# Optimization experiments

Hardware: AMD Instinct MI355X
Metric: run time of the kernel (lower is better)

The kernel has to match this reference:

```python
import jax, jax.numpy as jnp
import numpy as np

EPS = 1e-7
N_NODES = 100000

# --- Lorentz model (c = 1), working at the origin o = (1, 0, ..., 0) ---

def expmap0(v_spatial):
    """Exp map at origin: tangent spatial part [N, d] -> hyperboloid point [N, d+1]."""
    nrm = jnp.sqrt(jnp.maximum(jnp.sum(v_spatial * v_spatial, axis=-1, keepdims=True), EPS))
    x0 = jnp.cosh(nrm)
    xs = jnp.sinh(nrm) / nrm * v_spatial
    return jnp.concatenate([x0, xs], axis=-1)


def logmap0(x):
    """Log map at origin: point [N, d+1] -> tangent spatial part [N, d]."""
    x0 = jnp.maximum(x[..., :1], 1.0 + EPS)
    xs = x[..., 1:]
    nrm = jnp.sqrt(jnp.maximum(jnp.sum(xs * xs, axis=-1, keepdims=True), EPS))
    return jnp.arccosh(x0) / nrm * xs


def sigmoid_nonlin(x):
    # log map -> sigmoid in tangent space -> exp map (c_in = c_out = 1)
    return expmap0(jax.nn.sigmoid(logmap0(x)))


def hgcn_layer(x, edge_index, W, b):
    """HGCN conv: tangent-space linear + mean aggregation over edges + exp map."""
    t = logmap0(x)                      # [N, d_in]
    h = t @ W + b                       # [N, d_out]
    src, dst = edge_index[0], edge_index[1]
    msg = h[src]                        # [E, d_out] gather
    agg = jax.ops.segment_sum(msg, dst, num_segments=N_NODES)
    deg = jax.ops.segment_sum(jnp.ones((edge_index.shape[1],), h.dtype), dst,
                              num_segments=N_NODES)
    agg = agg / jnp.maximum(deg, 1.0)[:, None]
    return expmap0(agg)


def setup_inputs() -> dict:
    key = jax.random.key(0)
    ks = jax.random.split(key, 10)
    d_in, h1, h2, h_mlp, d_out = 64, 64, 64, 128, 40
    return {
        "features": jax.random.normal(ks[0], (N_NODES, d_in), jnp.float32),
        "edge_index": jax.random.randint(ks[1], (2, 1600000), 0, N_NODES, jnp.int64),
        "W1": jax.random.normal(ks[2], (d_in, h1), jnp.float32) * 0.05,
        "b1": jnp.zeros((h1,), jnp.float32),
        "W2": jax.random.normal(ks[3], (h1, h2), jnp.float32) * 0.05,
        "b2": jnp.zeros((h2,), jnp.float32),
        "W3": jax.random.normal(ks[4], (h2, h_mlp), jnp.float32) * 0.05,
        "b3": jnp.zeros((h_mlp,), jnp.float32),
        "W4": jax.random.normal(ks[5], (h_mlp, d_out), jnp.float32) * 0.05,
        "b4": jnp.zeros((d_out,), jnp.float32),
    }


def reference(features, edge_index, W1, b1, W2, b2, W3, b3, W4, b4):
    # lift Euclidean features to the hyperboloid (pad time coord, exp map)
    x = expmap0(features)                       # [N, d_in+1]
    x = hgcn_layer(x, edge_index, W1, b1)
    x = sigmoid_nonlin(x)
    x = hgcn_layer(x, edge_index, W2, b2)
    x = sigmoid_nonlin(x)
    t = logmap0(x)                              # [N, h2] (spatial part, drops time coord)
    # MLP head (dropout inactive at eval)
    h = jax.nn.relu(t @ W3 + b3)
    return h @ W4 + b4
```

## Files before the change

### kernel.cpp

```cpp
#include <hip/hip_runtime.h>


constexpr int CSHIFT = 9;
constexpr int CNODES = 1 << CSHIFT;
constexpr int EPB    = 4096;
constexpr int EPT    = EPB / 256;
constexpr int CAP    = 16384;

constexpr int W1_OFF = 0;
constexpr int W2_OFF = 64 * 72;
constexpr int W3_OFF = W2_OFF + 64 * 72;
constexpr int W4_OFF = W3_OFF + 128 * 72;
constexpr int WIMG_TOT = W4_OFF + 48 * 136;
constexpr int W234_SH = WIMG_TOT - W2_OFF;

typedef __attribute__((ext_vector_type(8))) short short8;
typedef __attribute__((ext_vector_type(4))) float floatx4;

__device__ __forceinline__ float sigmoidf(float x) {
    return 1.0f / (1.0f + __expf(-x));
}
__device__ __forceinline__ unsigned short f2bf(float f) {
    unsigned int u = __float_as_uint(f);
    u = (u + 0x7FFFu + ((u >> 16) & 1u)) >> 16;
    return (unsigned short)u;
}

__global__ __launch_bounds__(256) void cast_k(const float* __restrict__ in,
                                              unsigned short* __restrict__ out,
                                              int n8) {
    int i = blockIdx.x * 256 + threadIdx.x;
    if (i >= n8) return;
    const float4* p = (const float4*)in + (size_t)i * 2;
    float4 a = p[0], b = p[1];
    uint4 o;
    o.x = (unsigned)f2bf(a.x) | ((unsigned)f2bf(a.y) << 16);
    o.y = (unsigned)f2bf(a.z) | ((unsigned)f2bf(a.w) << 16);
    o.z = (unsigned)f2bf(b.x) | ((unsigned)f2bf(b.y) << 16);
    o.w = (unsigned)f2bf(b.z) | ((unsigned)f2bf(b.w) << 16);
    ((uint4*)out)[i] = o;
}

__global__ __launch_bounds__(256) void prep_k(const float* __restrict__ W1,
                                              const float* __restrict__ W2,
                                              const float* __restrict__ W3,
                                              const float* __restrict__ W4,
                                              unsigned short* __restrict__ img) {
    int i = blockIdx.x * 256 + threadIdx.x;
    if (i >= WIMG_TOT) return;
    float v = 0.f;
    if (i < W2_OFF) {
        int j = i, n = j / 72, k = j % 72;
        if (k < 64) v = W1[k * 64 + n];
    } else if (i < W3_OFF) {
        int j = i - W2_OFF, n = j / 72, k = j % 72;
        if (k < 64) v = W2[k * 64 + n];
    } else if (i < W4_OFF) {
        int j = i - W3_OFF, n = j / 72, k = j % 72;
        if (k < 64) v = W3[k * 128 + n];
    } else {
        int j = i - W4_OFF, n = j / 136, k = j % 136;
        if (n < 40 && k < 128) v = W4[k * 40 + n];
    }
    img[i] = f2bf(v);
}

__global__ __launch_bounds__(256) void part_a(const int* __restrict__ src,
                                              const int* __restrict__ dst,
                                              int* __restrict__ ccur,
                                              int* __restrict__ arena,
                                              int E, int NBUCK) {
    __shared__ int  hist[256];
    __shared__ int  exoff[256];
    __shared__ int  lcur[256];
    __shared__ int  gbase[256];
    __shared__ int  stage[EPB];
    __shared__ unsigned char stageB[EPB];

    const int tid = threadIdx.x;
    const int e0  = blockIdx.x * EPB;
    const int ec  = min(EPB, E - e0);

    int pk[EPT], bk[EPT];
    hist[tid] = 0;
    __syncthreads();
    #pragma unroll
    for (int j = 0; j < EPT; j++) {
        int idx = tid + j * 256;
        if (idx < ec) {
            int s = src[e0 + idx];
            int d = dst[e0 + idx];
            bk[j] = d >> CSHIFT;
            pk[j] = s | ((d & (CNODES - 1)) << 17);
            atomicAdd(&hist[bk[j]], 1);
        } else bk[j] = -1;
    }
    __syncthreads();
    const int h = hist[tid];
    exoff[tid] = h;
    __syncthreads();
    for (int dd = 1; dd < 256; dd <<= 1) {
        int v = 0;
        if (tid >= dd) v = exoff[tid - dd];
        __syncthreads();
        if (tid >= dd) exoff[tid] += v;
        __syncthreads();
    }
    const int ex = exoff[tid] - h;
    int gb = 0;
    if (tid < NBUCK && h > 0) gb = atomicAdd(ccur + tid, h);
    __syncthreads();
    exoff[tid] = ex;
    lcur[tid]  = ex;
    gbase[tid] = gb;
    __syncthreads();
    #pragma unroll
    for (int j = 0; j < EPT; j++) {
        if (bk[j] >= 0) {
            int l = atomicAdd(&lcur[bk[j]], 1);
            stage[l]  = pk[j];
            stageB[l] = (unsigned char)bk[j];
        }
    }
    __syncthreads();
    for (int i = tid; i < ec; i += 256) {
        int b = stageB[i];
        arena[(size_t)b * CAP + gbase[b] + (i - exoff[b])] = stage[i];
    }
}

__global__ __launch_bounds__(256) void scanc_k(const int* __restrict__ ccur,
                                               int* __restrict__ coff,
                                               int* __restrict__ offN,
                                               int NBUCK, int E) {
    __shared__ int sh[256];
    const int tid = threadIdx.x;
    sh[tid] = (tid < NBUCK) ? ccur[tid] : 0;
    __syncthreads();
    for (int d = 1; d < 256; d <<= 1) {
        int v = 0;
        if (tid >= d) v = sh[tid - d];
        __syncthreads();
        if (tid >= d) sh[tid] += v;
        __syncthreads();
    }
    if (tid < NBUCK) coff[tid] = (tid > 0) ? sh[tid - 1] : 0;
    if (tid == 0) { coff[NBUCK] = E; *offN = E; }
}

__global__ __launch_bounds__(256) void csr_fine(const int* __restrict__ arena,
                                                const int* __restrict__ coff,
                                                int* __restrict__ off,
                                                int* __restrict__ ssrc, int N) {
    __shared__ int cnt[CNODES];
    __shared__ int cur[CNODES];
    __shared__ int part[256];
    const int b = blockIdx.x;
    const int node0 = b << CSHIFT;
    const int cbeg = coff[b];
    const int ec   = coff[b + 1] - cbeg;
    const int* pe  = arena + (size_t)b * CAP;
    const int tid = threadIdx.x;

    cnt[tid] = 0;
    cnt[tid + 256] = 0;
    __syncthreads();
    for (int i = tid; i < ec; i += 256)
        atomicAdd(&cnt[(pe[i] >> 17) & (CNODES - 1)], 1);
    __syncthreads();
    const int c0 = cnt[2 * tid], c1 = cnt[2 * tid + 1];
    part[tid] = c0 + c1;
    __syncthreads();
    for (int d = 1; d < 256; d <<= 1) {
        int v = 0;
        if (tid >= d) v = part[tid - d];
        __syncthreads();
        if (tid >= d) part[tid] += v;
        __syncthreads();
    }
    const int ex = (tid > 0) ? part[tid - 1] : 0;
    cur[2 * tid]     = ex;
    cur[2 * tid + 1] = ex + c0;
    if (node0 + 2 * tid     < N) off[node0 + 2 * tid]     = cbeg + ex;
    if (node0 + 2 * tid + 1 < N) off[node0 + 2 * tid + 1] = cbeg + ex + c0;
    __syncthreads();
    for (int i = tid; i < ec; i += 256) {
        int p = pe[i];
        int pos = cbeg + atomicAdd(&cur[(p >> 17) & (CNODES - 1)], 1);
        ssrc[pos] = p & 0x1FFFF;
    }
}

#define ACC8(v)                                    \
    acc[0] += __uint_as_float((v).x << 16);        \
    acc[1] += __uint_as_float((v).x & 0xFFFF0000u);\
    acc[2] += __uint_as_float((v).y << 16);        \
    acc[3] += __uint_as_float((v).y & 0xFFFF0000u);\
    acc[4] += __uint_as_float((v).z << 16);        \
    acc[5] += __uint_as_float((v).z & 0xFFFF0000u);\
    acc[6] += __uint_as_float((v).w << 16);        \
    acc[7] += __uint_as_float((v).w & 0xFFFF0000u);

__global__ __launch_bounds__(256) void agg_k(const unsigned short* __restrict__ h,
                                             const int* __restrict__ off,
                                             const int* __restrict__ ssrc,
                                             unsigned short* __restrict__ outb,
                                             int N) {
    int t = blockIdx.x * 256 + threadIdx.x;
    int g = t >> 3;
    if (g >= N) return;
    int q = (t & 7) * 8;
    int beg = off[g], end = off[g + 1];
    float acc[8] = {0.f, 0.f, 0.f, 0.f, 0.f, 0.f, 0.f, 0.f};
    int i = beg;
    for (; i + 4 <= end; i += 4) {
        int s0 = ssrc[i], s1 = ssrc[i + 1], s2 = ssrc[i + 2], s3 = ssrc[i + 3];
        uint4 v0 = *(const uint4*)(h + (size_t)s0 * 64 + q);
        uint4 v1 = *(const uint4*)(h + (size_t)s1 * 64 + q);
        uint4 v2 = *(const uint4*)(h + (size_t)s2 * 64 + q);
        uint4 v3 = *(const uint4*)(h + (size_t)s3 * 64 + q);
        ACC8(v0); ACC8(v1); ACC8(v2); ACC8(v3);
    }
    for (; i < end; i++) {
        int s = ssrc[i];
        uint4 v = *(const uint4*)(h + (size_t)s * 64 + q);
        ACC8(v);
    }
    float inv = 1.0f / (float)max(end - beg, 1);
    uint4 p;
    p.x = (unsigned)f2bf(acc[0] * inv) | ((unsigned)f2bf(acc[1] * inv) << 16);
    p.y = (unsigned)f2bf(acc[2] * inv) | ((unsigned)f2bf(acc[3] * inv) << 16);
    p.z = (unsigned)f2bf(acc[4] * inv) | ((unsigned)f2bf(acc[5] * inv) << 16);
    p.w = (unsigned)f2bf(acc[6] * inv) | ((unsigned)f2bf(acc[7] * inv) << 16);
    *(uint4*)(outb + (size_t)g * 64 + q) = p;
}

__global__ __launch_bounds__(256) void gemmsig_k(
    const unsigned short* __restrict__ Abf, const int* __restrict__ off,
    const unsigned short* __restrict__ img, const float* __restrict__ bias,
    unsigned short* __restrict__ out, int N)
{
    __shared__ alignas(16) unsigned short WT[64 * 72];
    __shared__ float bs[64];
    __shared__ unsigned char dz[64];

    const int tid = threadIdx.x;
    const int rowB = blockIdx.x * 64;
    {
        const uint4* s = (const uint4*)(img + W1_OFF);
        uint4* d = (uint4*)WT;
        #pragma unroll
        for (int i = 0; i < 3; i++) {
            int idx = tid + i * 256;
            if (idx < 576) d[idx] = s[idx];
        }
    }
    if (tid < 64) {
        bs[tid] = bias[tid];
        int row = rowB + tid;
        dz[tid] = (row < N) ? (off[row + 1] == off[row]) : 0;
    }
    __syncthreads();

    const int w = tid >> 6, lane = tid & 63;
    const int m = lane & 15, quad = lane >> 4;
    const int row0 = rowB + w * 16;
    const int arow = min(row0 + m, N - 1);

    floatx4 acc[4];
    #pragma unroll
    for (int c = 0; c < 4; c++) acc[c] = (floatx4){0.f, 0.f, 0.f, 0.f};
    #pragma unroll
    for (int kk = 0; kk < 64; kk += 32) {
        short8 a = *(const short8*)(Abf + (size_t)arow * 64 + kk + quad * 8);
        #pragma unroll
        for (int c = 0; c < 4; c++) {
            short8 b = *(const short8*)(WT + (c * 16 + m) * 72 + kk + quad * 8);
            acc[c] = __builtin_amdgcn_mfma_f32_16x16x32_bf16(a, b, acc[c], 0, 0, 0);
        }
    }
    #pragma unroll
    for (int c = 0; c < 4; c++) {
        int col = c * 16 + m;
        #pragma unroll
        for (int r = 0; r < 4; r++) {
            int rl = w * 16 + quad * 4 + r;
            int row = rowB + rl;
            if (row < N) {
                float v = dz[rl] ? 0.5f : sigmoidf(acc[c][r] + bs[col]);
                out[(size_t)row * 64 + col] = f2bf(v);
            }
        }
    }
}

__global__ __launch_bounds__(256) void ep3b_k(
    const unsigned short* __restrict__ Abf, const int* __restrict__ off,
    const unsigned short* __restrict__ img,
    const float* __restrict__ b2, const float* __restrict__ b3,
    const float* __restrict__ b4, float* __restrict__ out, int N)
{
    __shared__ alignas(16) unsigned short W234[W234_SH];
    __shared__ alignas(16) unsigned short T2[64 * 72];
    __shared__ alignas(16) unsigned short H3[64 * 136];
    __shared__ float b2s[64], b3s[128], b4s[48];
    __shared__ unsigned char dz[64];

    const unsigned short* W2T = W234;
    const unsigned short* W3T = W234 + 64 * 72;
    const unsigned short* W4T = W234 + 64 * 72 + 128 * 72;

    const int tid = threadIdx.x;
    const int rowB = blockIdx.x * 64;
    {
        const uint4* s = (const uint4*)(img + W2_OFF);
        uint4* d = (uint4*)W234;
        for (int i = tid; i < W234_SH / 8; i += 256) d[i] = s[i];
    }
    if (tid < 64) {
        b2s[tid] = b2[tid];
        int row = rowB + tid;
        dz[tid] = (row < N) ? (off[row + 1] == off[row]) : 0;
    }
    if (tid < 128) b3s[tid] = b3[tid];
    if (tid < 48)  b4s[tid] = (tid < 40) ? b4[tid] : 0.f;
    __syncthreads();

    const int w = tid >> 6, lane = tid & 63;
    const int m = lane & 15, quad = lane >> 4;
    const int row0 = rowB + w * 16;

    {
        floatx4 acc[4];
        #pragma unroll
        for (int c = 0; c < 4; c++) acc[c] = (floatx4){0.f, 0.f, 0.f, 0.f};
        const int arow = min(row0 + m, N - 1);
        #pragma unroll
        for (int kk = 0; kk < 64; kk += 32) {
            short8 a = *(const short8*)(Abf + (size_t)arow * 64 + kk + quad * 8);
            #pragma unroll
            for (int c = 0; c < 4; c++) {
                short8 b = *(const short8*)(W2T + (c * 16 + m) * 72 + kk + quad * 8);
                acc[c] = __builtin_amdgcn_mfma_f32_16x16x32_bf16(a, b, acc[c], 0, 0, 0);
            }
        }
        #pragma unroll
        for (int c = 0; c < 4; c++) {
            int col = c * 16 + m;
            #pragma unroll
            for (int r = 0; r < 4; r++) {
                int rl = w * 16 + quad * 4 + r;
                float v = dz[rl] ? 0.5f : sigmoidf(acc[c][r] + b2s[col]);
                T2[rl * 72 + col] = f2bf(v);
            }
        }
    }
    __syncthreads();

    {
        floatx4 acc[8];
        #pragma unroll
        for (int c = 0; c < 8; c++) acc[c] = (floatx4){0.f, 0.f, 0.f, 0.f};
        #pragma unroll
        for (int kk = 0; kk < 64; kk += 32) {
            short8 a = *(const short8*)(T2 + (w * 16 + m) * 72 + kk + quad * 8);
            #pragma unroll
            for (int c = 0; c < 8; c++) {
                short8 b = *(const short8*)(W3T + (c * 16 + m) * 72 + kk + quad * 8);
                acc[c] = __builtin_amdgcn_mfma_f32_16x16x32_bf16(a, b, acc[c], 0, 0, 0);
            }
        }
        #pragma unroll
        for (int c = 0; c < 8; c++) {
            int col = c * 16 + m;
            #pragma unroll
            for (int r = 0; r < 4; r++) {
                int rl = w * 16 + quad * 4 + r;
                H3[rl * 136 + col] = f2bf(fmaxf(acc[c][r] + b3s[col], 0.f));
            }
        }
    }
    __syncthreads();

    {
        floatx4 acc[3];
        #pragma unroll
        for (int c = 0; c < 3; c++) acc[c] = (floatx4){0.f, 0.f, 0.f, 0.f};
        #pragma unroll
        for (int kk = 0; kk < 128; kk += 32) {
            short8 a = *(const short8*)(H3 + (w * 16 + m) * 136 + kk + quad * 8);
            #pragma unroll
            for (int c = 0; c < 3; c++) {
                short8 b = *(const short8*)(W4T + (c * 16 + m) * 136 + kk + quad * 8);
                acc[c] = __builtin_amdgcn_mfma_f32_16x16x32_bf16(a, b, acc[c], 0, 0, 0);
            }
        }
        #pragma unroll
        for (int c = 0; c < 3; c++) {
            int col = c * 16 + m;
            if (col < 40) {
                #pragma unroll
                for (int r = 0; r < 4; r++) {
                    int row = row0 + quad * 4 + r;
                    if (row < N) out[(size_t)row * 40 + col] = acc[c][r] + b4s[col];
                }
            }
        }
    }
}

extern "C" void kernel_launch(void* const* d_in, const int* in_sizes, int n_in,
                              void* d_out, int out_size, void* d_ws, size_t ws_size,
                              hipStream_t stream)
{
    const float* feat = (const float*)d_in[0];
    const int*   eidx = (const int*)d_in[1];
    const float* W1 = (const float*)d_in[2];
    const float* b1 = (const float*)d_in[3];
    const float* W2 = (const float*)d_in[4];
    const float* b2 = (const float*)d_in[5];
    const float* W3 = (const float*)d_in[6];
    const float* b3 = (const float*)d_in[7];
    const float* W4 = (const float*)d_in[8];
    const float* b4 = (const float*)d_in[9];

    const int N = in_sizes[0] / 64;
    const int E = in_sizes[1] / 2;
    const int* src = eidx;
    const int* dst = eidx + E;

    const int NBUCK = (N + CNODES - 1) / CNODES;

    unsigned short* featbf = (unsigned short*)d_ws;
    unsigned short* t1     = featbf + (size_t)N * 64;
    unsigned short* aggF   = t1     + (size_t)N * 64;
    unsigned short* img    = aggF   + (size_t)N * 64;
    int*   off   = (int*)(img + ((WIMG_TOT + 7) & ~7));
    int*   ccur  = off + (N + 1);
    int*   coff  = ccur + NBUCK;
    int*   ssrc  = coff + (NBUCK + 1);
    int*   arena = ssrc + E;
    float* out   = (float*)d_out;

    hipMemsetAsync(ccur, 0, (size_t)NBUCK * sizeof(int), stream);

    const dim3 blk(256);
    const int gP  = (E + EPB - 1) / EPB;
    const int g64 = (N + 63) / 64;
    const int gC  = (N * 64 / 8 + 255) / 256;
    const int gW  = (WIMG_TOT + 255) / 256;
    const int gAg = (int)(((size_t)N * 8 + 255) / 256);

    cast_k<<<gC, blk, 0, stream>>>(feat, featbf, N * 64 / 8);
    prep_k<<<gW, blk, 0, stream>>>(W1, W2, W3, W4, img);
    part_a<<<gP, blk, 0, stream>>>(src, dst, ccur, arena, E, NBUCK);
    scanc_k<<<1, blk, 0, stream>>>(ccur, coff, off + N, NBUCK, E);
    csr_fine<<<NBUCK, blk, 0, stream>>>(arena, coff, off, ssrc, N);

    agg_k<<<gAg, blk, 0, stream>>>(featbf, off, ssrc, aggF, N);
    gemmsig_k<<<g64, blk, 0, stream>>>(aggF, off, img, b1, t1, N);
    agg_k<<<gAg, blk, 0, stream>>>(t1, off, ssrc, aggF, N);
    ep3b_k<<<g64, blk, 0, stream>>>(aggF, off, img, b2, b3, b4, out, N);
}
```

Measured before the change: 246.1 us.

## Merge prep kernels, fold bucket scan into CSR build, pre-swizzle MFMA weights

The feature cast and weight prep now run as one kernel, and the bucket-offset scan is folded into every csr_fine block, which removes two launches. Weights are stored in an MFMA fragment-ready layout and read straight from global memory, so the GEMM kernels no longer stage weights, biases and zero-degree flags in LDS or sync before the first MFMA. The aggregation loop is unrolled to 8 gathers per step with a 2-wide tail to keep more loads in flight. In exchange, every csr_fine block repeats the small scan and the GEMMs depend on L1/L2 hits for their weight reads.

```diff
diff --git a/kernel.cpp b/kernel.cpp
--- a/kernel.cpp
+++ b/kernel.cpp
@@ -7,12 +7,11 @@
 constexpr int EPT    = EPB / 256;
 constexpr int CAP    = 16384;
 
-constexpr int W1_OFF = 0;
-constexpr int W2_OFF = 64 * 72;
-constexpr int W3_OFF = W2_OFF + 64 * 72;
-constexpr int W4_OFF = W3_OFF + 128 * 72;
-constexpr int WIMG_TOT = W4_OFF + 48 * 136;
-constexpr int W234_SH = WIMG_TOT - W2_OFF;
+constexpr int W1F_OFF = 0;
+constexpr int W2F_OFF = 4096;
+constexpr int W3F_OFF = 8192;
+constexpr int W4F_OFF = 16384;
+constexpr int WIMG_TOT = 22528;
 
 typedef __attribute__((ext_vector_type(8))) short short8;
 typedef __attribute__((ext_vector_type(4))) float floatx4;
@@ -26,43 +25,46 @@
     return (unsigned short)u;
 }
 
-__global__ __launch_bounds__(256) void cast_k(const float* __restrict__ in,
-                                              unsigned short* __restrict__ out,
-                                              int n8) {
+__global__ __launch_bounds__(256) void prep_cast_k(
+    const float* __restrict__ feat, unsigned short* __restrict__ featbf,
+    const float* __restrict__ W1, const float* __restrict__ W2,
+    const float* __restrict__ W3, const float* __restrict__ W4,
+    unsigned short* __restrict__ img, int n8)
+{
     int i = blockIdx.x * 256 + threadIdx.x;
-    if (i >= n8) return;
-    const float4* p = (const float4*)in + (size_t)i * 2;
-    float4 a = p[0], b = p[1];
-    uint4 o;
-    o.x = (unsigned)f2bf(a.x) | ((unsigned)f2bf(a.y) << 16);
-    o.y = (unsigned)f2bf(a.z) | ((unsigned)f2bf(a.w) << 16);
-    o.z = (unsigned)f2bf(b.x) | ((unsigned)f2bf(b.y) << 16);
-    o.w = (unsigned)f2bf(b.z) | ((unsigned)f2bf(b.w) << 16);
-    ((uint4*)out)[i] = o;
-}
-
-__global__ __launch_bounds__(256) void prep_k(const float* __restrict__ W1,
-                                              const float* __restrict__ W2,
-                                              const float* __restrict__ W3,
-                                              const float* __restrict__ W4,
-                                              unsigned short* __restrict__ img) {
-    int i = blockIdx.x * 256 + threadIdx.x;
-    if (i >= WIMG_TOT) return;
+    if (i < n8) {
+        const float4* p = (const float4*)feat + (size_t)i * 2;
+        float4 a = p[0], b = p[1];
+        uint4 o;
+        o.x = (unsigned)f2bf(a.x) | ((unsigned)f2bf(a.y) << 16);
+        o.y = (unsigned)f2bf(a.z) | ((unsigned)f2bf(a.w) << 16);
+        o.z = (unsigned)f2bf(b.x) | ((unsigned)f2bf(b.y) << 16);
+        o.w = (unsigned)f2bf(b.z) | ((unsigned)f2bf(b.w) << 16);
+        ((uint4*)featbf)[i] = o;
+        return;
+    }
+    int t = i - n8;
+    if (t >= WIMG_TOT) return;
     float v = 0.f;
-    if (i < W2_OFF) {
-        int j = i, n = j / 72, k = j % 72;
-        if (k < 64) v = W1[k * 64 + n];
-    } else if (i < W3_OFF) {
-        int j = i - W2_OFF, n = j / 72, k = j % 72;
-        if (k < 64) v = W2[k * 64 + n];
-    } else if (i < W4_OFF) {
-        int j = i - W3_OFF, n = j / 72, k = j % 72;
-        if (k < 64) v = W3[k * 128 + n];
+    int s = t;
+    if (s < W2F_OFF) {
+        int j = s & 7, m = (s >> 3) & 15, q = (s >> 7) & 3, kk = (s >> 9) & 1, c = s >> 10;
+        v = W1[(kk * 32 + q * 8 + j) * 64 + c * 16 + m];
+    } else if (s < W3F_OFF) {
+        s -= W2F_OFF;
+        int j = s & 7, m = (s >> 3) & 15, q = (s >> 7) & 3, kk = (s >> 9) & 1, c = s >> 10;
+        v = W2[(kk * 32 + q * 8 + j) * 64 + c * 16 + m];
+    } else if (s < W4F_OFF) {
+        s -= W3F_OFF;
+        int j = s & 7, m = (s >> 3) & 15, q = (s >> 7) & 3, kk = (s >> 9) & 1, c = s >> 10;
+        v = W3[(kk * 32 + q * 8 + j) * 128 + c * 16 + m];
     } else {
-        int j = i - W4_OFF, n = j / 136, k = j % 136;
-        if (n < 40 && k < 128) v = W4[k * 40 + n];
-    }
-    img[i] = f2bf(v);
+        s -= W4F_OFF;
+        int j = s & 7, m = (s >> 3) & 15, q = (s >> 7) & 3, kk = (s >> 9) & 3, c = s >> 11;
+        int n = c * 16 + m;
+        if (n < 40) v = W4[(kk * 32 + q * 8 + j) * 40 + n];
+    }
+    img[t] = f2bf(v);
 }
 
 __global__ __launch_bounds__(256) void part_a(const int* __restrict__ src,
@@ -129,39 +131,33 @@
     }
 }
 
-__global__ __launch_bounds__(256) void scanc_k(const int* __restrict__ ccur,
-                                               int* __restrict__ coff,
-                                               int* __restrict__ offN,
-                                               int NBUCK, int E) {
-    __shared__ int sh[256];
-    const int tid = threadIdx.x;
-    sh[tid] = (tid < NBUCK) ? ccur[tid] : 0;
-    __syncthreads();
-    for (int d = 1; d < 256; d <<= 1) {
-        int v = 0;
-        if (tid >= d) v = sh[tid - d];
-        __syncthreads();
-        if (tid >= d) sh[tid] += v;
-        __syncthreads();
-    }
-    if (tid < NBUCK) coff[tid] = (tid > 0) ? sh[tid - 1] : 0;
-    if (tid == 0) { coff[NBUCK] = E; *offN = E; }
-}
-
 __global__ __launch_bounds__(256) void csr_fine(const int* __restrict__ arena,
-                                                const int* __restrict__ coff,
+                                                const int* __restrict__ ccur,
                                                 int* __restrict__ off,
-                                                int* __restrict__ ssrc, int N) {
+                                                int* __restrict__ ssrc,
+                                                int N, int E, int NBUCK) {
     __shared__ int cnt[CNODES];
     __shared__ int cur[CNODES];
     __shared__ int part[256];
     const int b = blockIdx.x;
     const int node0 = b << CSHIFT;
-    const int cbeg = coff[b];
-    const int ec   = coff[b + 1] - cbeg;
-    const int* pe  = arena + (size_t)b * CAP;
     const int tid = threadIdx.x;
 
+    part[tid] = (tid < NBUCK) ? ccur[tid] : 0;
+    __syncthreads();
+    for (int d = 1; d < 256; d <<= 1) {
+        int v = 0;
+        if (tid >= d) v = part[tid - d];
+        __syncthreads();
+        if (tid >= d) part[tid] += v;
+        __syncthreads();
+    }
+    const int cbeg = (b > 0) ? part[b - 1] : 0;
+    const int ec   = ccur[b];
+    if (b == 0 && tid == 0) off[N] = E;
+    __syncthreads();
+
+    const int* pe = arena + (size_t)b * CAP;
     cnt[tid] = 0;
     cnt[tid + 256] = 0;
     __syncthreads();
@@ -213,17 +209,25 @@
     int beg = off[g], end = off[g + 1];
     float acc[8] = {0.f, 0.f, 0.f, 0.f, 0.f, 0.f, 0.f, 0.f};
     int i = beg;
-    for (; i + 4 <= end; i += 4) {
-        int s0 = ssrc[i], s1 = ssrc[i + 1], s2 = ssrc[i + 2], s3 = ssrc[i + 3];
-        uint4 v0 = *(const uint4*)(h + (size_t)s0 * 64 + q);
-        uint4 v1 = *(const uint4*)(h + (size_t)s1 * 64 + q);
-        uint4 v2 = *(const uint4*)(h + (size_t)s2 * 64 + q);
-        uint4 v3 = *(const uint4*)(h + (size_t)s3 * 64 + q);
+    for (; i + 8 <= end; i += 8) {
+        uint4 v0 = *(const uint4*)(h + (size_t)ssrc[i]     * 64 + q);
+        uint4 v1 = *(const uint4*)(h + (size_t)ssrc[i + 1] * 64 + q);
+        uint4 v2 = *(const uint4*)(h + (size_t)ssrc[i + 2] * 64 + q);
+        uint4 v3 = *(const uint4*)(h + (size_t)ssrc[i + 3] * 64 + q);
+        uint4 v4 = *(const uint4*)(h + (size_t)ssrc[i + 4] * 64 + q);
+        uint4 v5 = *(const uint4*)(h + (size_t)ssrc[i + 5] * 64 + q);
+        uint4 v6 = *(const uint4*)(h + (size_t)ssrc[i + 6] * 64 + q);
+        uint4 v7 = *(const uint4*)(h + (size_t)ssrc[i + 7] * 64 + q);
         ACC8(v0); ACC8(v1); ACC8(v2); ACC8(v3);
+        ACC8(v4); ACC8(v5); ACC8(v6); ACC8(v7);
+    }
+    for (; i + 2 <= end; i += 2) {
+        uint4 v0 = *(const uint4*)(h + (size_t)ssrc[i]     * 64 + q);
+        uint4 v1 = *(const uint4*)(h + (size_t)ssrc[i + 1] * 64 + q);
+        ACC8(v0); ACC8(v1);
     }
     for (; i < end; i++) {
-        int s = ssrc[i];
-        uint4 v = *(const uint4*)(h + (size_t)s * 64 + q);
+        uint4 v = *(const uint4*)(h + (size_t)ssrc[i] * 64 + q);
         ACC8(v);
     }
     float inv = 1.0f / (float)max(end - beg, 1);
@@ -240,55 +244,42 @@
     const unsigned short* __restrict__ img, const float* __restrict__ bias,
     unsigned short* __restrict__ out, int N)
 {
-    __shared__ alignas(16) unsigned short WT[64 * 72];
-    __shared__ float bs[64];
-    __shared__ unsigned char dz[64];
-
     const int tid = threadIdx.x;
     const int rowB = blockIdx.x * 64;
-    {
-        const uint4* s = (const uint4*)(img + W1_OFF);
-        uint4* d = (uint4*)WT;
-        #pragma unroll
-        for (int i = 0; i < 3; i++) {
-            int idx = tid + i * 256;
-            if (idx < 576) d[idx] = s[idx];
-        }
-    }
-    if (tid < 64) {
-        bs[tid] = bias[tid];
-        int row = rowB + tid;
-        dz[tid] = (row < N) ? (off[row + 1] == off[row]) : 0;
-    }
-    __syncthreads();
-
     const int w = tid >> 6, lane = tid & 63;
     const int m = lane & 15, quad = lane >> 4;
     const int row0 = rowB + w * 16;
     const int arow = min(row0 + m, N - 1);
+    const short8* Wf = (const short8*)(img + W1F_OFF);
 
     floatx4 acc[4];
     #pragma unroll
     for (int c = 0; c < 4; c++) acc[c] = (floatx4){0.f, 0.f, 0.f, 0.f};
     #pragma unroll
-    for (int kk = 0; kk < 64; kk += 32) {
-        short8 a = *(const short8*)(Abf + (size_t)arow * 64 + kk + quad * 8);
+    for (int kk = 0; kk < 2; kk++) {
+        short8 a = *(const short8*)(Abf + (size_t)arow * 64 + kk * 32 + quad * 8);
         #pragma unroll
         for (int c = 0; c < 4; c++) {
-            short8 b = *(const short8*)(WT + (c * 16 + m) * 72 + kk + quad * 8);
+            short8 b = Wf[((c * 2 + kk) * 4 + quad) * 16 + m];
             acc[c] = __builtin_amdgcn_mfma_f32_16x16x32_bf16(a, b, acc[c], 0, 0, 0);
         }
+    }
+    bool dzr[4];
+    int rows[4];
+    #pragma unroll
+    for (int r = 0; r < 4; r++) {
+        rows[r] = row0 + quad * 4 + r;
+        dzr[r] = (rows[r] < N) ? (off[rows[r] + 1] == off[rows[r]]) : false;
     }
     #pragma unroll
     for (int c = 0; c < 4; c++) {
         int col = c * 16 + m;
+        float bv = bias[col];
         #pragma unroll
         for (int r = 0; r < 4; r++) {
-            int rl = w * 16 + quad * 4 + r;
-            int row = rowB + rl;
-            if (row < N) {
-                float v = dz[rl] ? 0.5f : sigmoidf(acc[c][r] + bs[col]);
-                out[(size_t)row * 64 + col] = f2bf(v);
+            if (rows[r] < N) {
+                float v = dzr[r] ? 0.5f : sigmoidf(acc[c][r] + bv);
+                out[(size_t)rows[r] * 64 + col] = f2bf(v);
             }
         }
     }
@@ -300,57 +291,44 @@
     const float* __restrict__ b2, const float* __restrict__ b3,
     const float* __restrict__ b4, float* __restrict__ out, int N)
 {
-    __shared__ alignas(16) unsigned short W234[W234_SH];
     __shared__ alignas(16) unsigned short T2[64 * 72];
     __shared__ alignas(16) unsigned short H3[64 * 136];
-    __shared__ float b2s[64], b3s[128], b4s[48];
-    __shared__ unsigned char dz[64];
-
-    const unsigned short* W2T = W234;
-    const unsigned short* W3T = W234 + 64 * 72;
-    const unsigned short* W4T = W234 + 64 * 72 + 128 * 72;
 
     const int tid = threadIdx.x;
     const int rowB = blockIdx.x * 64;
-    {
-        const uint4* s = (const uint4*)(img + W2_OFF);
-        uint4* d = (uint4*)W234;
-        for (int i = tid; i < W234_SH / 8; i += 256) d[i] = s[i];
-    }
-    if (tid < 64) {
-        b2s[tid] = b2[tid];
-        int row = rowB + tid;
-        dz[tid] = (row < N) ? (off[row + 1] == off[row]) : 0;
-    }
-    if (tid < 128) b3s[tid] = b3[tid];
-    if (tid < 48)  b4s[tid] = (tid < 40) ? b4[tid] : 0.f;
-    __syncthreads();
-
     const int w = tid >> 6, lane = tid & 63;
     const int m = lane & 15, quad = lane >> 4;
     const int row0 = rowB + w * 16;
 
     {
+        const short8* Wf = (const short8*)(img + W2F_OFF);
         floatx4 acc[4];
         #pragma unroll
         for (int c = 0; c < 4; c++) acc[c] = (floatx4){0.f, 0.f, 0.f, 0.f};
         const int arow = min(row0 + m, N - 1);
         #pragma unroll
-        for (int kk = 0; kk < 64; kk += 32) {
-            short8 a = *(const short8*)(Abf + (size_t)arow * 64 + kk + quad * 8);
+        for (int kk = 0; kk < 2; kk++) {
+            short8 a = *(const short8*)(Abf + (size_t)arow * 64 + kk * 32 + quad * 8);
             #pragma unroll
             for (int c = 0; c < 4; c++) {
-                short8 b = *(const short8*)(W2T + (c * 16 + m) * 72 + kk + quad * 8);
+                short8 b = Wf[((c * 2 + kk) * 4 + quad) * 16 + m];
                 acc[c] = __builtin_amdgcn_mfma_f32_16x16x32_bf16(a, b, acc[c], 0, 0, 0);
             }
+        }
+        bool dzr[4];
+        #pragma unroll
+        for (int r = 0; r < 4; r++) {
+            int row = row0 + quad * 4 + r;
+            dzr[r] = (row < N) ? (off[row + 1] == off[row]) : false;
         }
         #pragma unroll
         for (int c = 0; c < 4; c++) {
             int col = c * 16 + m;
+            float bv = b2[col];
             #pragma unroll
             for (int r = 0; r < 4; r++) {
                 int rl = w * 16 + quad * 4 + r;
-                float v = dz[rl] ? 0.5f : sigmoidf(acc[c][r] + b2s[col]);
+                float v = dzr[r] ? 0.5f : sigmoidf(acc[c][r] + bv);
                 T2[rl * 72 + col] = f2bf(v);
             }
         }
@@ -358,40 +336,43 @@
     __syncthreads();
 
     {
+        const short8* Wf = (const short8*)(img + W3F_OFF);
         floatx4 acc[8];
         #pragma unroll
         for (int c = 0; c < 8; c++) acc[c] = (floatx4){0.f, 0.f, 0.f, 0.f};
         #pragma unroll
-        for (int kk = 0; kk < 64; kk += 32) {
-            short8 a = *(const short8*)(T2 + (w * 16 + m) * 72 + kk + quad * 8);
+        for (int kk = 0; kk < 2; kk++) {
+            short8 a = *(const short8*)(T2 + (w * 16 + m) * 72 + kk * 32 + quad * 8);
             #pragma unroll
             for (int c = 0; c < 8; c++) {
-                short8 b = *(const short8*)(W3T + (c * 16 + m) * 72 + kk + quad * 8);
+                short8 b = Wf[((c * 2 + kk) * 4 + quad) * 16 + m];
                 acc[c] = __builtin_amdgcn_mfma_f32_16x16x32_bf16(a, b, acc[c], 0, 0, 0);
             }
         }
         #pragma unroll
         for (int c = 0; c < 8; c++) {
             int col = c * 16 + m;
+            float bv = b3[col];
             #pragma unroll
             for (int r = 0; r < 4; r++) {
                 int rl = w * 16 + quad * 4 + r;
-                H3[rl * 136 + col] = f2bf(fmaxf(acc[c][r] + b3s[col], 0.f));
+                H3[rl * 136 + col] = f2bf(fmaxf(acc[c][r] + bv, 0.f));
             }
         }
     }
     __syncthreads();
 
     {
+        const short8* Wf = (const short8*)(img + W4F_OFF);
         floatx4 acc[3];
         #pragma unroll
         for (int c = 0; c < 3; c++) acc[c] = (floatx4){0.f, 0.f, 0.f, 0.f};
         #pragma unroll
-        for (int kk = 0; kk < 128; kk += 32) {
-            short8 a = *(const short8*)(H3 + (w * 16 + m) * 136 + kk + quad * 8);
+        for (int kk = 0; kk < 4; kk++) {
+            short8 a = *(const short8*)(H3 + (w * 16 + m) * 136 + kk * 32 + quad * 8);
             #pragma unroll
             for (int c = 0; c < 3; c++) {
-                short8 b = *(const short8*)(W4T + (c * 16 + m) * 136 + kk + quad * 8);
+                short8 b = Wf[((c * 4 + kk) * 4 + quad) * 16 + m];
                 acc[c] = __builtin_amdgcn_mfma_f32_16x16x32_bf16(a, b, acc[c], 0, 0, 0);
             }
         }
@@ -399,10 +380,11 @@
         for (int c = 0; c < 3; c++) {
             int col = c * 16 + m;
             if (col < 40) {
+                float bv = b4[col];
                 #pragma unroll
                 for (int r = 0; r < 4; r++) {
                     int row = row0 + quad * 4 + r;
-                    if (row < N) out[(size_t)row * 40 + col] = acc[c][r] + b4s[col];
+                    if (row < N) out[(size_t)row * 40 + col] = acc[c][r] + bv;
                 }
             }
         }
@@ -435,10 +417,9 @@
     unsigned short* t1     = featbf + (size_t)N * 64;
     unsigned short* aggF   = t1     + (size_t)N * 64;
     unsigned short* img    = aggF   + (size_t)N * 64;
-    int*   off   = (int*)(img + ((WIMG_TOT + 7) & ~7));
+    int*   off   = (int*)(img + WIMG_TOT);
     int*   ccur  = off + (N + 1);
-    int*   coff  = ccur + NBUCK;
-    int*   ssrc  = coff + (NBUCK + 1);
+    int*   ssrc  = ccur + NBUCK;
     int*   arena = ssrc + E;
     float* out   = (float*)d_out;
 
@@ -447,15 +428,13 @@
     const dim3 blk(256);
     const int gP  = (E + EPB - 1) / EPB;
     const int g64 = (N + 63) / 64;
-    const int gC  = (N * 64 / 8 + 255) / 256;
-    const int gW  = (WIMG_TOT + 255) / 256;
+    const int n8  = N * 64 / 8;
+    const int gPC = (n8 + WIMG_TOT + 255) / 256;
     const int gAg = (int)(((size_t)N * 8 + 255) / 256);
 
-    cast_k<<<gC, blk, 0, stream>>>(feat, featbf, N * 64 / 8);
-    prep_k<<<gW, blk, 0, stream>>>(W1, W2, W3, W4, img);
+    prep_cast_k<<<gPC, blk, 0, stream>>>(feat, featbf, W1, W2, W3, W4, img, n8);
     part_a<<<gP, blk, 0, stream>>>(src, dst, ccur, arena, E, NBUCK);
-    scanc_k<<<1, blk, 0, stream>>>(ccur, coff, off + N, NBUCK, E);
-    csr_fine<<<NBUCK, blk, 0, stream>>>(arena, coff, off, ssrc, N);
+    csr_fine<<<NBUCK, blk, 0, stream>>>(arena, ccur, off, ssrc, N, E, NBUCK);
 
     agg_k<<<gAg, blk, 0, stream>>>(featbf, off, ssrc, aggF, N);
     gemmsig_k<<<g64, blk, 0, stream>>>(aggF, off, img, b1, t1, N);
```

Result: faster. 235.9 us (-4.2%).
